# Kernel tuning notes

Hardware: AMD Instinct MI355X
Metric: run time of the kernel (lower is better)

## Reference

```python
import jax, jax.numpy as jnp
import numpy as np

CENTER = 7          # center_size
K = 5               # neighbourhood_size
DIL = 1             # dilation
EPS_LN = 1e-5       # torch F.layer_norm default eps
EPS_COS = 1e-8      # torch F.cosine_similarity default eps


def _unfold_image(image, k):
    """torch F.unfold(image, k, stride=1, padding=k//2) -> [B, T, C*k*k]."""
    B, C, H, W = image.shape
    p = k // 2
    padded = jnp.pad(image, ((0, 0), (0, 0), (p, p), (p, p)))
    # channel-major patch layout (c, ki, kj), matching torch.unfold
    patches = jnp.stack([padded[:, :, i:i + H, j:j + W]
                         for i in range(k) for j in range(k)], axis=2)  # [B,C,k*k,H,W]
    return patches.reshape(B, C * k * k, H * W).transpose(0, 2, 1)       # [B,T,D]


def _neighbour_indices(H, W, k, dil):
    """generate_local_indices with constant padding value N=H*W, center removed -> [T, k*k-1]."""
    half = (k - 1) // 2 * dil
    N = H * W
    inds = np.arange(N).reshape(H, W)
    padded = np.full((H + 2 * half, W + 2 * half), N, dtype=np.int64)
    padded[half:half + H, half:half + W] = inds
    cols = [padded[i * dil:i * dil + H, j * dil:j * dil + W].reshape(-1)
            for i in range(k) for j in range(k)]
    local = np.stack(cols, axis=-1)  # [T, k*k]
    center = (k * k) // 2
    keep = [s for s in range(k * k) if s != center]
    return jnp.asarray(local[:, keep])  # [T, S], S = k*k-1


def setup_inputs() -> dict:
    key = jax.random.key(0)
    image = jax.random.uniform(key, (2, 3, 128, 128), dtype=jnp.float32)
    return {"image": image}


def reference(image):
    B, C, H, W = image.shape
    T = H * W
    kc = CENTER

    # im2col of center patches: [B, T, C*kc*kc]
    bu = _unfold_image(image, kc)

    # per-channel LayerNorm over kc*kc elements (no affine), then +1.0 twice
    bu = bu.reshape(B, T, C, kc * kc)
    mu = bu.mean(axis=-1, keepdims=True)
    var = ((bu - mu) ** 2).mean(axis=-1, keepdims=True)
    bu = (bu - mu) / jnp.sqrt(var + EPS_LN)
    bu = bu.reshape(B, T, C * kc * kc) + 2.0  # [B,T,D]

    # local neighbourhood indices (padding index == T marks out-of-bounds)
    nb = _neighbour_indices(H, W, K, DIL)  # [T, S]

    # gather surround patches; row T is the invalid (zero) row
    bu_ext = jnp.concatenate([bu, jnp.zeros((B, 1, bu.shape[-1]), bu.dtype)], axis=1)
    surround = bu_ext[:, nb]  # [B,T,S,D]

    # cosine similarity between each center patch and its S neighbours
    dot = jnp.einsum('btd,btsd->bts', bu, surround)
    n_node = jnp.linalg.norm(bu, axis=-1)        # [B,T]
    n_sur = jnp.linalg.norm(surround, axis=-1)   # [B,T,S]
    cos = dot / jnp.maximum(n_node[:, :, None] * n_sur, EPS_COS)
    dist = (1.0 - cos) * 0.5  # = 1 - (1+cos)/2

    # masked mean over valid neighbours
    mask = (nb != T).astype(dist.dtype)  # [T,S]
    sal = (dist * mask).sum(-1) / mask.sum(-1)
    return sal.reshape(B, H, W)
```

## Files before the change

### kernel.cpp

```cpp
#include <hip/hip_runtime.h>

#define HH 128
#define WW 128
#define TX 8
#define TY 8
#define IR 22
#define ISTR 25
#define S4 16
#define S4S 17
#define S2 12
#define S2S 13
#define PR 18
#define NTHR 256

__global__ void __launch_bounds__(NTHR)
err_kernel(const float* __restrict__ img, float* __restrict__ out) {
    __shared__ float s_img[3][IR][ISTR];
    __shared__ union U1 {
        float rs[2][3][IR][S4S];
        float H[36][PR][S2];
    } u1;
    __shared__ float s_mu[3][S4][S4S];
    __shared__ float s_r [3][S4][S4S];
    __shared__ union U2 {
        float nsq[3][S2][S2S];
        float part[12][S2][S2S];
    } u2;
    __shared__ float s_rnrm[S2][S2S];
    __shared__ float s_B[12][3][S2][S2S];
    __shared__ float s_red[2][4][64];

    const int tid = threadIdx.x;
    const int x0 = blockIdx.x * TX, y0 = blockIdx.y * TY;
    const float* imgb = img + (size_t)blockIdx.z * 3 * HH * WW;

    for (int i = tid; i < 3 * IR * IR; i += NTHR) {
        const int c = i / (IR * IR);
        const int rem = i - c * IR * IR;
        const int iy = rem / IR, ix = rem - iy * IR;
        const int yy = y0 - 7 + iy, xx = x0 - 7 + ix;
        float v = 0.f;
        if ((unsigned)yy < HH && (unsigned)xx < WW)
            v = imgb[c * HH * WW + yy * WW + xx];
        s_img[c][iy][ix] = v;
    }
    __syncthreads();

    if (tid < 66) {
        const int c = tid / 22, row = tid - c * 22;
        float f[22];
#pragma unroll
        for (int j = 0; j < 22; ++j) f[j] = s_img[c][row][j];
        float s = 0.f, s2 = 0.f;
#pragma unroll
        for (int k = 0; k < 7; ++k) { s += f[k]; s2 = fmaf(f[k], f[k], s2); }
        u1.rs[0][c][row][0] = s; u1.rs[1][c][row][0] = s2;
#pragma unroll
        for (int x = 1; x < S4; ++x) {
            s += f[x + 6] - f[x - 1];
            s2 += fmaf(f[x + 6], f[x + 6], -f[x - 1] * f[x - 1]);
            u1.rs[0][c][row][x] = s; u1.rs[1][c][row][x] = s2;
        }
    }
    __syncthreads();

    if (tid < 96) {
        const int c = tid / 32;
        const int rem = tid - c * 32;
        const int col = rem >> 1, h = rem & 1;
        const int r0 = h * 8;
        float s = 0.f, s2 = 0.f;
#pragma unroll
        for (int k = 0; k < 7; ++k) { s += u1.rs[0][c][r0 + k][col]; s2 += u1.rs[1][c][r0 + k][col]; }
#pragma unroll
        for (int i = 0; i < 8; ++i) {
            const int rr4 = r0 + i;
            const float mu  = s * (1.f / 49.f);
            const float var = fmaxf(fmaf(-mu, mu, s2 * (1.f / 49.f)), 0.f);
            const float rv  = rsqrtf(var + 1e-5f);
            s_mu[c][rr4][col] = mu;
            s_r [c][rr4][col] = rv;
            const int sr = rr4 - 2, sc = col - 2;
            if ((unsigned)sr < S2 && (unsigned)sc < S2)
                u2.nsq[c][sr][sc] = fmaf(49.f * var, rv * rv, 196.f);
            if (i < 7) {
                s  += u1.rs[0][c][rr4 + 7][col] - u1.rs[0][c][rr4][col];
                s2 += u1.rs[1][c][rr4 + 7][col] - u1.rs[1][c][rr4][col];
            }
        }
    }
    __syncthreads();

    if (tid < 144) {
        const int py = tid / 12, px = tid - py * 12;
        s_rnrm[py][px] = rsqrtf(u2.nsq[0][py][px] + u2.nsq[1][py][px] + u2.nsq[2][py][px]);
    }
    for (int q = tid; q < 648; q += NTHR) {
        const int cd = q / 18;
        const int prow = q - cd * 18;
        const int dI = cd / 3, c = cd - dI * 3;
        const int u = dI + 13;
        const int dy = u / 5 - 2, dx = u - (u / 5) * 5 - 2;
        const float* rowA = &s_img[c][prow + 2][2];
        const float* rowB = &s_img[c][prow + 2 + dy][2 + dx];
        float P[18];
#pragma unroll
        for (int j = 0; j < 18; ++j) P[j] = rowA[j] * rowB[j];
        float hsum = P[0] + P[1] + P[2] + P[3] + P[4] + P[5] + P[6];
        u1.H[cd][prow][0] = hsum;
#pragma unroll
        for (int j = 1; j < S2; ++j) { hsum += P[j + 6] - P[j - 1]; u1.H[cd][prow][j] = hsum; }
    }
    __syncthreads();

    for (int q = tid; q < 432; q += NTHR) {
        const int cd = q / 12, col = q - cd * 12;
        const int dI = cd / 3, c = cd - dI * 3;
        float b = 0.f;
#pragma unroll
        for (int k = 0; k < 7; ++k) b += u1.H[cd][k][col];
        s_B[dI][c][0][col] = b;
#pragma unroll
        for (int r2 = 1; r2 < S2; ++r2) {
            b += u1.H[cd][r2 + 6][col] - u1.H[cd][r2 - 1][col];
            s_B[dI][c][r2][col] = b;
        }
    }
    __syncthreads();

    for (int q = tid; q < 1728; q += NTHR) {
        const int dI = q / 144;
        const int pos = q - dI * 144;
        const int py = pos / 12, px = pos - py * 12;
        const int u = dI + 13;
        const int dy = u / 5 - 2, dx = u - (u / 5) * 5 - 2;
        const int r1 = py + 2, c1 = px + 2;
        const int r2 = r1 + dy, c2 = c1 + dx;
        float acc = 0.f;
#pragma unroll
        for (int c = 0; c < 3; ++c) {
            const float m = s_mu[c][r1][c1] * s_mu[c][r2][c2];
            const float v = fmaf(-49.f, m, s_B[dI][c][py][px]);
            acc = fmaf(v, s_r[c][r1][c1] * s_r[c][r2][c2], acc);
        }
        u2.part[dI][py][px] = acc;
    }
    __syncthreads();

    {
        const int p = tid & 63, quarter = tid >> 6;
        const int ty = p >> 3, tx = p & 7;
        const int gy = y0 + ty, gx = x0 + tx;
        float acc = 0.f, cnt = 0.f;
#pragma unroll
        for (int j = 0; j < 3; ++j) {
            const int dI = quarter * 3 + j;
            const int u = dI + 13;
            const int dy = u / 5 - 2, dx = u - (u / 5) * 5 - 2;
            if ((unsigned)(gy + dy) < HH && (unsigned)(gx + dx) < WW) {
                const float ps = u2.part[dI][ty + 2][tx + 2];
                acc = fmaf(588.f + ps, s_rnrm[ty + 2 + dy][tx + 2 + dx], acc);
                cnt += 1.f;
            }
            if ((unsigned)(gy - dy) < HH && (unsigned)(gx - dx) < WW) {
                const float ps = u2.part[dI][ty + 2 - dy][tx + 2 - dx];
                acc = fmaf(588.f + ps, s_rnrm[ty + 2 - dy][tx + 2 - dx], acc);
                cnt += 1.f;
            }
        }
        s_red[0][quarter][p] = acc;
        s_red[1][quarter][p] = cnt;
    }
    __syncthreads();
    if (tid < 64) {
        const int ty = tid >> 3, tx = tid & 7;
        const float a = s_red[0][0][tid] + s_red[0][1][tid] + s_red[0][2][tid] + s_red[0][3][tid];
        const float n = s_red[1][0][tid] + s_red[1][1][tid] + s_red[1][2][tid] + s_red[1][3][tid];
        const float rn = s_rnrm[ty + 2][tx + 2];
        out[(size_t)blockIdx.z * HH * WW + (y0 + ty) * WW + (x0 + tx)] =
            0.5f - a * rn / (2.f * n);
    }
}

extern "C" void kernel_launch(void* const* d_in, const int* in_sizes, int n_in,
                              void* d_out, int out_size, void* d_ws, size_t ws_size,
                              hipStream_t stream) {
    const float* img = (const float*)d_in[0];
    float* out = (float*)d_out;
    dim3 grid(WW / TX, HH / TY, 2);
    dim3 block(NTHR);
    hipLaunchKernelGGL(err_kernel, grid, block, 0, stream, img, out);
}
```

Baseline: 14.86 us.

## Fuse vertical box-sum with correlation stage and drop final cross-thread reduction

Merges the vertical sliding-window sum and the per-position normalized correlation into one stage: each of 144 threads keeps running 3-channel sums in registers and writes part directly, removing the s_B shared buffer and one barrier. The final neighbour accumulation is done by 64 threads looping over all 12 offsets, removing the s_red reduction buffer and another barrier. Image smem stride changes from 25 to 23. This lowers shared memory use and synchronisation, but leaves fewer threads active per stage, so each thread does a longer serial chain.

After: 14.38 us. -3.2%, faster.

```diff
diff --git a/kernel.cpp b/kernel.cpp
--- a/kernel.cpp
+++ b/kernel.cpp
@@ -5,12 +5,11 @@
 #define TX 8
 #define TY 8
 #define IR 22
-#define ISTR 25
+#define ISTR 23
 #define S4 16
 #define S4S 17
 #define S2 12
 #define S2S 13
-#define PR 18
 #define NTHR 256
 
 __global__ void __launch_bounds__(NTHR)
@@ -18,7 +17,7 @@
     __shared__ float s_img[3][IR][ISTR];
     __shared__ union U1 {
         float rs[2][3][IR][S4S];
-        float H[36][PR][S2];
+        float H[36][18][S2];
     } u1;
     __shared__ float s_mu[3][S4][S4S];
     __shared__ float s_r [3][S4][S4S];
@@ -27,8 +26,6 @@
         float part[12][S2][S2S];
     } u2;
     __shared__ float s_rnrm[S2][S2S];
-    __shared__ float s_B[12][3][S2][S2S];
-    __shared__ float s_red[2][4][64];
 
     const int tid = threadIdx.x;
     const int x0 = blockIdx.x * TX, y0 = blockIdx.y * TY;
@@ -113,48 +110,44 @@
     }
     __syncthreads();
 
-    for (int q = tid; q < 432; q += NTHR) {
-        const int cd = q / 12, col = q - cd * 12;
-        const int dI = cd / 3, c = cd - dI * 3;
-        float b = 0.f;
+    if (tid < 144) {
+        const int dI = tid / 12, col = tid - dI * 12;
+        const int u = dI + 13;
+        const int dy = u / 5 - 2, dx = u - (u / 5) * 5 - 2;
+        float B[3];
 #pragma unroll
-        for (int k = 0; k < 7; ++k) b += u1.H[cd][k][col];
-        s_B[dI][c][0][col] = b;
+        for (int c = 0; c < 3; ++c) {
+            float b = 0.f;
 #pragma unroll
-        for (int r2 = 1; r2 < S2; ++r2) {
-            b += u1.H[cd][r2 + 6][col] - u1.H[cd][r2 - 1][col];
-            s_B[dI][c][r2][col] = b;
+            for (int k = 0; k < 7; ++k) b += u1.H[dI * 3 + c][k][col];
+            B[c] = b;
+        }
+#pragma unroll
+        for (int y = 0; y < S2; ++y) {
+            float acc = 0.f;
+#pragma unroll
+            for (int c = 0; c < 3; ++c) {
+                const float m = s_mu[c][y + 2][col + 2] * s_mu[c][y + 2 + dy][col + 2 + dx];
+                const float v = fmaf(-49.f, m, B[c]);
+                acc = fmaf(v, s_r[c][y + 2][col + 2] * s_r[c][y + 2 + dy][col + 2 + dx], acc);
+            }
+            u2.part[dI][y][col] = acc;
+            if (y < S2 - 1) {
+#pragma unroll
+                for (int c = 0; c < 3; ++c)
+                    B[c] += u1.H[dI * 3 + c][y + 7][col] - u1.H[dI * 3 + c][y][col];
+            }
         }
     }
     __syncthreads();
 
-    for (int q = tid; q < 1728; q += NTHR) {
-        const int dI = q / 144;
-        const int pos = q - dI * 144;
-        const int py = pos / 12, px = pos - py * 12;
-        const int u = dI + 13;
-        const int dy = u / 5 - 2, dx = u - (u / 5) * 5 - 2;
-        const int r1 = py + 2, c1 = px + 2;
-        const int r2 = r1 + dy, c2 = c1 + dx;
-        float acc = 0.f;
-#pragma unroll
-        for (int c = 0; c < 3; ++c) {
-            const float m = s_mu[c][r1][c1] * s_mu[c][r2][c2];
-            const float v = fmaf(-49.f, m, s_B[dI][c][py][px]);
-            acc = fmaf(v, s_r[c][r1][c1] * s_r[c][r2][c2], acc);
-        }
-        u2.part[dI][py][px] = acc;
-    }
-    __syncthreads();
-
-    {
-        const int p = tid & 63, quarter = tid >> 6;
-        const int ty = p >> 3, tx = p & 7;
+    if (tid < 64) {
+        const int ty = tid >> 3, tx = tid & 7;
         const int gy = y0 + ty, gx = x0 + tx;
+        const float rnt = s_rnrm[ty + 2][tx + 2];
         float acc = 0.f, cnt = 0.f;
 #pragma unroll
-        for (int j = 0; j < 3; ++j) {
-            const int dI = quarter * 3 + j;
+        for (int dI = 0; dI < 12; ++dI) {
             const int u = dI + 13;
             const int dy = u / 5 - 2, dx = u - (u / 5) * 5 - 2;
             if ((unsigned)(gy + dy) < HH && (unsigned)(gx + dx) < WW) {
@@ -168,17 +161,7 @@
                 cnt += 1.f;
             }
         }
-        s_red[0][quarter][p] = acc;
-        s_red[1][quarter][p] = cnt;
-    }
-    __syncthreads();
-    if (tid < 64) {
-        const int ty = tid >> 3, tx = tid & 7;
-        const float a = s_red[0][0][tid] + s_red[0][1][tid] + s_red[0][2][tid] + s_red[0][3][tid];
-        const float n = s_red[1][0][tid] + s_red[1][1][tid] + s_red[1][2][tid] + s_red[1][3][tid];
-        const float rn = s_rnrm[ty + 2][tx + 2];
-        out[(size_t)blockIdx.z * HH * WW + (y0 + ty) * WW + (x0 + tx)] =
-            0.5f - a * rn / (2.f * n);
+        out[(size_t)blockIdx.z * HH * WW + gy * WW + gx] = 0.5f - acc * rnt / (2.f * cnt);
     }
 }
 
```
